# Kernel tuning notes

Measured on AMD Instinct MI355X. Metric: run time of the kernel, lower is better.

Reference implementation:

```python
import jax, jax.numpy as jnp
import numpy as np

B, S, T = 128, 128, 128
E, H = 256, 512
NEG_INF = -1e9


def setup_inputs() -> dict:
    key = jax.random.key(0)
    ks = jax.random.split(key, 12)
    rn = lambda k, sh: (jax.random.normal(k, sh, jnp.float32) * 0.05)
    return {
        "trg_embed": rn(ks[0], (B, T, E)),
        "encoder_hidden": rn(ks[1], (B, S, 2 * H)),
        "encoder_final": rn(ks[2], (1, B, 2 * H)),
        "src_mask": jnp.ones((B, 1, S), bool),
        "trg_mask": jnp.ones((B, T), bool),
        # Bahdanau attention params (Linear, bias=False)
        "W_key": rn(ks[3], (H, 2 * H)),      # key_layer
        "W_query": rn(ks[4], (H, H)),        # query_layer
        "v_energy": rn(ks[5], (H,)),         # energy_layer (H -> 1)
        # GRU cell params (torch layout: gates [r, z, n])
        "W_ih": rn(ks[6], (3 * H, E + 2 * H)),
        "W_hh": rn(ks[7], (3 * H, H)),
        "b_ih": rn(ks[8], (3 * H,)),
        "b_hh": rn(ks[9], (3 * H,)),
        # bridge: Linear(2H -> H, bias=True)
        "W_bridge": rn(ks[10], (H, 2 * H)),
        "b_bridge": jnp.zeros((H,), jnp.float32),
        # pre_output_layer: Linear(H + 2H + E -> H, bias=False)
        "W_preout": rn(ks[11], (H, H + 2 * H + E)),
    }


def reference(trg_embed, encoder_hidden, encoder_final, src_mask, trg_mask,
              W_key, W_query, v_energy, W_ih, W_hh, b_ih, b_hh,
              W_bridge, b_bridge, W_preout):
    # proj_key precomputed once, as in the torch module
    proj_key = jnp.einsum("bsk,hk->bsh", encoder_hidden, W_key)  # [B,S,H]
    # init_hidden: tanh(bridge(encoder_final)); num_layers=1 -> h: [B,H]
    h0 = jnp.tanh(encoder_final[0] @ W_bridge.T + b_bridge)
    mask = src_mask[:, 0, :]  # [B,S]

    def step(h, prev_embed):  # h: [B,H], prev_embed: [B,E]
        # Bahdanau additive attention, query = last-layer hidden
        q = h @ W_query.T  # [B,H]
        scores = jnp.einsum("bsh,h->bs", jnp.tanh(q[:, None, :] + proj_key), v_energy)
        scores = jnp.where(mask, scores, NEG_INF)
        alphas = jax.nn.softmax(scores, axis=-1)
        context = jnp.einsum("bs,bsd->bd", alphas, encoder_hidden)  # [B,2H]
        # single-step GRU (torch gate order r, z, n)
        x = jnp.concatenate([prev_embed, context], axis=-1)  # [B,E+2H]
        gi = x @ W_ih.T + b_ih
        gh = h @ W_hh.T + b_hh
        i_r, i_z, i_n = jnp.split(gi, 3, axis=-1)
        h_r, h_z, h_n = jnp.split(gh, 3, axis=-1)
        r = jax.nn.sigmoid(i_r + h_r)
        z = jax.nn.sigmoid(i_z + h_z)
        n = jnp.tanh(i_n + r * h_n)
        h_new = (1.0 - z) * n + z * h
        # pre-output projection (dropout p=0 / eval mode)
        pre = jnp.concatenate([prev_embed, h_new, context], axis=-1) @ W_preout.T
        return h_new, (h_new, pre)

    xs = jnp.swapaxes(trg_embed, 0, 1)  # [T,B,E]
    hT, (states, preouts) = jax.lax.scan(step, h0, xs)
    decoder_states = jnp.swapaxes(states, 0, 1)      # [B,T,H]
    pre_output_vectors = jnp.swapaxes(preouts, 0, 1)  # [B,T,H]
    hidden = hT[None]  # [1,B,H] to mirror torch layout
    cell_state = jnp.zeros_like(hidden)  # GRU: untouched zeros
    return decoder_states, hidden, pre_output_vectors, cell_state
```

## Files before the change

kernel.cpp:

```cpp
#include <hip/hip_runtime.h>
#include <hip/hip_bf16.h>

typedef __bf16 bf16_t;
typedef __bf16 bf16x8 __attribute__((ext_vector_type(8)));
typedef float  f32x4  __attribute__((ext_vector_type(4)));
typedef float  f32x2  __attribute__((ext_vector_type(2)));

#define Bx 128
#define Sx 128
#define Tx 128
#define Ex 256
#define Hx 512
#define H2 1024
#define G3 1536
#define KX 1280
#define KP 1792

#define OUT_STATES 0
#define OUT_HID    8388608
#define OUT_PRE    8454144
#define OUT_CELL   16842752

__device__ __forceinline__ float fast_tanh(float x){
  float e = __expf(2.0f*x);
  return 1.0f - 2.0f/(e + 1.0f);
}
__device__ __forceinline__ float fast_sigmoid(float x){
  return 1.0f/(1.0f + __expf(-x));
}

__device__ __forceinline__ bf16x8 ld_cvt8(const float* p){
  f32x4 a = *(const f32x4*)p;
  f32x4 b = *(const f32x4*)(p+4);
  bf16x8 r;
  r[0]=(bf16_t)a[0]; r[1]=(bf16_t)a[1]; r[2]=(bf16_t)a[2]; r[3]=(bf16_t)a[3];
  r[4]=(bf16_t)b[0]; r[5]=(bf16_t)b[1]; r[6]=(bf16_t)b[2]; r[7]=(bf16_t)b[3];
  return r;
}

__device__ __forceinline__ f32x4 gemm_tile_bb(const bf16_t* A, int lda,
                                              const bf16_t* W, int ldw, int K, int lane){
  const int quad = lane >> 4, c = lane & 15;
  const bf16_t* pa = A + c*lda + quad*8;
  const bf16_t* pb = W + c*ldw + quad*8;
  f32x4 acc = {0.f,0.f,0.f,0.f};
  for (int k = 0; k < K; k += 32)
    acc = __builtin_amdgcn_mfma_f32_16x16x32_bf16(*(const bf16x8*)(pa+k),
                                                  *(const bf16x8*)(pb+k), acc, 0, 0, 0);
  return acc;
}

__device__ __forceinline__ void store_tile_f32(float* C, int ldc, f32x4 acc, int lane){
  const int quad = lane >> 4, c = lane & 15;
  #pragma unroll
  for (int r = 0; r < 4; r++) C[(quad*4 + r)*ldc + c] = acc[r];
}

__global__ void cvt_kernel(const float* __restrict__ in, bf16_t* __restrict__ out, int n){
  const int i = (blockIdx.x*256 + threadIdx.x)*4;
  if (i < n){
    f32x4 v = *(const f32x4*)(in + i);
    bf16_t o[4]; o[0]=(bf16_t)v[0]; o[1]=(bf16_t)v[1]; o[2]=(bf16_t)v[2]; o[3]=(bf16_t)v[3];
    *(ulong1*)(out + i) = *(ulong1*)o;
  }
}

__global__ void bridge_kernel(const float* __restrict__ ef, const float* __restrict__ Wb,
                              const float* __restrict__ bb,
                              float* __restrict__ hf, bf16_t* __restrict__ hb){
  const int b = blockIdx.x;
  const int h = threadIdx.x;
  __shared__ float efs[H2];
  for (int k = threadIdx.x; k < H2; k += blockDim.x) efs[k] = ef[b*H2 + k];
  __syncthreads();
  const float* wrow = Wb + h*H2;
  float acc = bb[h];
  for (int k = 0; k < H2; k += 4){
    f32x4 w = *(const f32x4*)(wrow + k);
    acc += efs[k]*w[0] + efs[k+1]*w[1] + efs[k+2]*w[2] + efs[k+3]*w[3];
  }
  float v = fast_tanh(acc);
  hf[b*Hx + h] = v;
  hb[b*Hx + h] = (bf16_t)v;
}

__global__ void pk_gemm(const float* __restrict__ eh, const bf16_t* __restrict__ Wkb,
                        bf16_t* __restrict__ pk){
  const int gwid = (blockIdx.x*blockDim.x + threadIdx.x) >> 6;
  const int lane = threadIdx.x & 63;
  const int quad = lane >> 4, c = lane & 15;
  const int mt = gwid >> 5;
  const int nt = gwid & 31;
  const float*  pa = eh  + (mt*16 + c)*H2 + quad*8;
  const bf16_t* pb = Wkb + (nt*16 + c)*H2 + quad*8;
  f32x4 acc = {0.f,0.f,0.f,0.f};
  for (int k = 0; k < H2; k += 32)
    acc = __builtin_amdgcn_mfma_f32_16x16x32_bf16(ld_cvt8(pa + k),
                                                  *(const bf16x8*)(pb + k), acc, 0,0,0);
  bf16_t* C = pk + mt*16*Hx + nt*16;
  #pragma unroll
  for (int r = 0; r < 4; r++) C[(quad*4 + r)*Hx + c] = (bf16_t)acc[r];
}

__global__ void __launch_bounds__(256)
p1_kernel(const bf16_t* __restrict__ hb, const bf16_t* __restrict__ Wqb,
          const bf16_t* __restrict__ Whhb, float* __restrict__ qf, float* __restrict__ ghf){
  const int lane = threadIdx.x & 63;
  const int gw = blockIdx.x*4 + (threadIdx.x >> 6);
  if (gw < 256){
    const int mt = gw >> 5, nt = gw & 31;
    f32x4 acc = gemm_tile_bb(hb + mt*16*Hx, Hx, Wqb + nt*16*Hx, Hx, Hx, lane);
    store_tile_f32(qf + mt*16*Hx + nt*16, Hx, acc, lane);
  } else {
    const int idx = gw - 256;
    const int mt = idx/96, nt = idx%96;
    f32x4 acc = gemm_tile_bb(hb + mt*16*Hx, Hx, Whhb + nt*16*Hx, Hx, Hx, lane);
    store_tile_f32(ghf + mt*16*G3 + nt*16, G3, acc, lane);
  }
}

__global__ void __launch_bounds__(256)
p2_kernel(const float* __restrict__ trg, const float* __restrict__ eh,
          const float* __restrict__ ven, const bf16_t* __restrict__ pk,
          const float* __restrict__ qf, bf16_t* __restrict__ xbuf, int t){
  const int tid  = threadIdx.x;
  const int lane = tid & 63;
  const int wid  = tid >> 6;
  const int b    = blockIdx.x >> 1;
  const int half = blockIdx.x & 1;

  __shared__ float sc[Sx];
  __shared__ float smax_s, ssum_s;

  float qv[8], vv[8];
  #pragma unroll
  for (int i = 0; i < 8; i++){
    qv[i] = qf[b*Hx + i*64 + lane];
    vv[i] = ven[i*64 + lane];
  }
  for (int j = 0; j < 32; j++){
    const int s = wid*32 + j;
    const bf16_t* row = pk + (b*Sx + s)*Hx;
    float p = 0.f;
    #pragma unroll
    for (int i = 0; i < 8; i++)
      p += fast_tanh(qv[i] + (float)row[i*64 + lane])*vv[i];
    #pragma unroll
    for (int o = 32; o; o >>= 1) p += __shfl_xor(p, o, 64);
    if (lane == 0) sc[s] = p;
  }
  __syncthreads();
  if (tid < 64){
    float m = fmaxf(sc[tid], sc[tid+64]);
    #pragma unroll
    for (int o = 32; o; o >>= 1) m = fmaxf(m, __shfl_xor(m, o, 64));
    if (tid == 0) smax_s = m;
  }
  __syncthreads();
  if (tid < 128) sc[tid] = __expf(sc[tid] - smax_s);
  __syncthreads();
  if (tid < 64){
    float ssum = sc[tid] + sc[tid+64];
    #pragma unroll
    for (int o = 32; o; o >>= 1) ssum += __shfl_xor(ssum, o, 64);
    if (tid == 0) ssum_s = ssum;
  }
  __syncthreads();
  const float inv = 1.0f/ssum_s;
  const int d0 = half*Hx + tid*2;
  const float* ehb = eh + b*Sx*H2;
  float c0 = 0.f, c1 = 0.f;
  #pragma unroll 4
  for (int s = 0; s < Sx; s++){
    const float a = sc[s];
    f32x2 v = *(const f32x2*)(ehb + s*H2 + d0);
    c0 += a*v[0];
    c1 += a*v[1];
  }
  c0 *= inv; c1 *= inv;
  bf16_t cb[2]; cb[0] = (bf16_t)c0; cb[1] = (bf16_t)c1;
  *(uint1*)(xbuf + b*KX + Ex + d0) = *(uint1*)cb;
  if (half == 0) xbuf[b*KX + tid] = (bf16_t)trg[(b*Tx + t)*Ex + tid];
}

__global__ void __launch_bounds__(256)
p3_kernel(const bf16_t* __restrict__ Wihb, const float* __restrict__ bih,
          const float* __restrict__ bhh, const bf16_t* __restrict__ Wpb,
          const bf16_t* __restrict__ xbuf, const float* __restrict__ ghf,
          float* __restrict__ hf, bf16_t* __restrict__ hb,
          float* __restrict__ states, float* __restrict__ pre, int t){
  const int lane = threadIdx.x & 63;
  const int gw = blockIdx.x*4 + (threadIdx.x >> 6);
  const int quad = lane >> 4, c16 = lane & 15;

  if (gw < 256){
    const int mt = gw >> 5, ntp = gw & 31;
    const bf16_t* A  = xbuf + (mt*16 + c16)*KX + quad*8;
    const bf16_t* B0 = Wihb + (ntp*16 + c16)*KX + quad*8;
    const bf16_t* B1 = B0 + Hx*KX;
    const bf16_t* B2 = B0 + H2*KX;
    f32x4 ar = {0.f,0.f,0.f,0.f}, az = ar, an = ar;
    for (int k = 0; k < KX; k += 32){
      bf16x8 a = *(const bf16x8*)(A + k);
      ar = __builtin_amdgcn_mfma_f32_16x16x32_bf16(a, *(const bf16x8*)(B0+k), ar, 0,0,0);
      az = __builtin_amdgcn_mfma_f32_16x16x32_bf16(a, *(const bf16x8*)(B1+k), az, 0,0,0);
      an = __builtin_amdgcn_mfma_f32_16x16x32_bf16(a, *(const bf16x8*)(B2+k), an, 0,0,0);
    }
    const int j = ntp*16 + c16;
    const float bir = bih[j], biz = bih[Hx+j], bin = bih[H2+j];
    const float bhr = bhh[j], bhz = bhh[Hx+j], bhn = bhh[H2+j];
    #pragma unroll
    for (int r = 0; r < 4; r++){
      const int b_ = mt*16 + quad*4 + r;
      const float hr = ghf[b_*G3 + j]       + bhr;
      const float hz = ghf[b_*G3 + Hx + j]  + bhz;
      const float hn = ghf[b_*G3 + H2 + j]  + bhn;
      const float rg = fast_sigmoid(ar[r] + bir + hr);
      const float zg = fast_sigmoid(az[r] + biz + hz);
      const float ng = fast_tanh(an[r] + bin + rg*hn);
      const float hold = hf[b_*Hx + j];
      const float hnew = (1.0f - zg)*ng + zg*hold;
      hf[b_*Hx + j] = hnew;
      hb[b_*Hx + j] = (bf16_t)hnew;
      states[(b_*Tx + t)*Hx + j] = hnew;
    }
  } else {
    const int idx = gw - 256;
    const int mt2 = idx >> 5, nt2 = idx & 31;
    const bf16_t* A = xbuf + (mt2*16 + c16)*KX + Ex + quad*8;
    const bf16_t* B = Wpb + (nt2*16 + c16)*KP + (Ex + Hx) + quad*8;
    f32x4 acc = {0.f,0.f,0.f,0.f};
    for (int k = 0; k < H2; k += 32)
      acc = __builtin_amdgcn_mfma_f32_16x16x32_bf16(*(const bf16x8*)(A+k),
                                                    *(const bf16x8*)(B+k), acc, 0,0,0);
    #pragma unroll
    for (int r = 0; r < 4; r++){
      const int b_ = mt2*16 + quad*4 + r;
      pre[(b_*Tx + t)*Hx + nt2*16 + c16] = acc[r];
    }
  }
}

__global__ void preout_gemm(const bf16_t* __restrict__ trgb, const float* __restrict__ states,
                            const bf16_t* __restrict__ Wpb, float* __restrict__ pre){
  const int gwid = (blockIdx.x*blockDim.x + threadIdx.x) >> 6;
  const int lane = threadIdx.x & 63;
  const int quad = lane >> 4, c16 = lane & 15;
  const int mt = gwid >> 5, nt = gwid & 31;
  const int m = mt*16 + c16;
  const bf16_t* Bp = Wpb + (nt*16 + c16)*KP + quad*8;
  f32x4 acc = {0.f,0.f,0.f,0.f};
  const bf16_t* Ae = trgb + m*Ex + quad*8;
  for (int k = 0; k < Ex; k += 32)
    acc = __builtin_amdgcn_mfma_f32_16x16x32_bf16(*(const bf16x8*)(Ae+k),
                                                  *(const bf16x8*)(Bp+k), acc, 0,0,0);
  const float* As = states + m*Hx + quad*8;
  for (int k = 0; k < Hx; k += 32)
    acc = __builtin_amdgcn_mfma_f32_16x16x32_bf16(ld_cvt8(As+k),
                                                  *(const bf16x8*)(Bp+Ex+k), acc, 0,0,0);
  float* C = pre + mt*16*Hx + nt*16;
  #pragma unroll
  for (int r = 0; r < 4; r++){
    const int o = (quad*4 + r)*Hx + c16;
    C[o] = acc[r] + C[o];
  }
}

__global__ void finalize_kernel(const float* __restrict__ hf,
                                float* __restrict__ hid, float* __restrict__ cell){
  const int i = blockIdx.x*256 + threadIdx.x;
  hid[i]  = hf[i];
  cell[i] = 0.0f;
}

extern "C" void kernel_launch(void* const* d_in, const int* in_sizes, int n_in,
                              void* d_out, int out_size, void* d_ws, size_t ws_size,
                              hipStream_t stream){
  int shift = 0;
  for (int i = 0; i < n_in; i++){
    if (in_sizes[i] == 1966080){ shift = i - 8; break; }
  }
  #define IN(k) (((k) < 3) ? d_in[(k)] : d_in[(k) + shift])
  const float* trg = (const float*)IN(0);
  const float* eh  = (const float*)IN(1);
  const float* ef  = (const float*)IN(2);
  const float* Wk  = (const float*)IN(5);
  const float* Wq  = (const float*)IN(6);
  const float* ven = (const float*)IN(7);
  const float* Wih = (const float*)IN(8);
  const float* Whh = (const float*)IN(9);
  const float* bih = (const float*)IN(10);
  const float* bhh = (const float*)IN(11);
  const float* Wb  = (const float*)IN(12);
  const float* bb  = (const float*)IN(13);
  const float* Wp  = (const float*)IN(14);
  #undef IN

  char* ws = (char*)d_ws;
  bf16_t* xbuf = (bf16_t*)(ws + 0);
  float*  hf   = (float* )(ws + 327680);
  bf16_t* hb   = (bf16_t*)(ws + 589824);
  float*  qf   = (float* )(ws + 720896);
  float*  ghf  = (float* )(ws + 983040);
  bf16_t* Wkb  = (bf16_t*)(ws + 1769472);
  bf16_t* Wqb  = (bf16_t*)(ws + 2818048);
  bf16_t* Whhb = (bf16_t*)(ws + 3342336);
  bf16_t* Wihb = (bf16_t*)(ws + 4915200);
  bf16_t* Wpb  = (bf16_t*)(ws + 8847360);
  bf16_t* trgb = (bf16_t*)(ws + 10682368);
  bf16_t* pk   = (bf16_t*)(ws + 19070976);

  float* out    = (float*)d_out;
  float* states = out + OUT_STATES;
  float* hid    = out + OUT_HID;
  float* pre    = out + OUT_PRE;
  float* cell   = out + OUT_CELL;

  cvt_kernel<<<dim3(512),  dim3(256), 0, stream>>>(Wk,  Wkb,  524288);
  cvt_kernel<<<dim3(256),  dim3(256), 0, stream>>>(Wq,  Wqb,  262144);
  cvt_kernel<<<dim3(768),  dim3(256), 0, stream>>>(Whh, Whhb, 786432);
  cvt_kernel<<<dim3(1920), dim3(256), 0, stream>>>(Wih, Wihb, 1966080);
  cvt_kernel<<<dim3(896),  dim3(256), 0, stream>>>(Wp,  Wpb,  917504);
  cvt_kernel<<<dim3(4096), dim3(256), 0, stream>>>(trg, trgb, 4194304);

  bridge_kernel<<<dim3(Bx), dim3(Hx), 0, stream>>>(ef, Wb, bb, hf, hb);
  pk_gemm<<<dim3(8192), dim3(256), 0, stream>>>(eh, Wkb, pk);

  for (int t = 0; t < Tx; t++){
    p1_kernel<<<dim3(256), dim3(256), 0, stream>>>(hb, Wqb, Whhb, qf, ghf);
    p2_kernel<<<dim3(256), dim3(256), 0, stream>>>(trg, eh, ven, pk, qf, xbuf, t);
    p3_kernel<<<dim3(128), dim3(256), 0, stream>>>(Wihb, bih, bhh, Wpb, xbuf, ghf,
                                                   hf, hb, states, pre, t);
  }

  preout_gemm<<<dim3(8192), dim3(256), 0, stream>>>(trgb, states, Wpb, pre);
  finalize_kernel<<<dim3(256), dim3(256), 0, stream>>>(hf, hid, cell);
}
```

Baseline: 9.220 ms.

## Fuse per-timestep kernels into one persistent kernel with grid-wide barriers

Replaces the 384 per-step kernel launches (three phases across 128 timesteps) with a single persistent kernel of 256 blocks. The blocks step through all timesteps and separate the phases with an atomic-counter grid barrier. This is meant to remove launch overhead and inter-kernel gaps in the latency-bound recurrence. It relies on all 256 blocks being co-resident, and it borrows the cell output buffer as barrier storage; finalize later overwrites that buffer.

```diff
diff --git a/kernel.cpp b/kernel.cpp
--- a/kernel.cpp
+++ b/kernel.cpp
@@ -15,6 +15,8 @@
 #define G3 1536
 #define KX 1280
 #define KP 1792
+
+#define NBLK 256
 
 #define OUT_STATES 0
 #define OUT_HID    8388608
@@ -55,6 +57,26 @@
   #pragma unroll
   for (int r = 0; r < 4; r++) C[(quad*4 + r)*ldc + c] = acc[r];
 }
+
+__device__ __forceinline__ void gsync(unsigned* barv, unsigned next){
+  __syncthreads();
+  if (threadIdx.x == 0){
+    unsigned prev = __hip_atomic_fetch_add(&barv[0], 1u, __ATOMIC_ACQ_REL,
+                                           __HIP_MEMORY_SCOPE_AGENT);
+    if (prev == (unsigned)(NBLK - 1)){
+      __hip_atomic_store(&barv[0], 0u, __ATOMIC_RELAXED, __HIP_MEMORY_SCOPE_AGENT);
+      __hip_atomic_store(&barv[1], next, __ATOMIC_RELEASE, __HIP_MEMORY_SCOPE_AGENT);
+    } else {
+      while (__hip_atomic_load(&barv[1], __ATOMIC_RELAXED,
+                               __HIP_MEMORY_SCOPE_AGENT) != next)
+        __builtin_amdgcn_s_sleep(2);
+      __builtin_amdgcn_fence(__ATOMIC_ACQUIRE, "agent");
+    }
+  }
+  __syncthreads();
+}
+
+__global__ void init_bar(unsigned* barv){ barv[0] = 0u; barv[1] = 0u; }
 
 __global__ void cvt_kernel(const float* __restrict__ in, bf16_t* __restrict__ out, int n){
   const int i = (blockIdx.x*256 + threadIdx.x)*4;
@@ -103,141 +125,145 @@
 }
 
 __global__ void __launch_bounds__(256)
-p1_kernel(const bf16_t* __restrict__ hb, const bf16_t* __restrict__ Wqb,
-          const bf16_t* __restrict__ Whhb, float* __restrict__ qf, float* __restrict__ ghf){
-  const int lane = threadIdx.x & 63;
-  const int gw = blockIdx.x*4 + (threadIdx.x >> 6);
-  if (gw < 256){
-    const int mt = gw >> 5, nt = gw & 31;
-    f32x4 acc = gemm_tile_bb(hb + mt*16*Hx, Hx, Wqb + nt*16*Hx, Hx, Hx, lane);
-    store_tile_f32(qf + mt*16*Hx + nt*16, Hx, acc, lane);
-  } else {
-    const int idx = gw - 256;
-    const int mt = idx/96, nt = idx%96;
-    f32x4 acc = gemm_tile_bb(hb + mt*16*Hx, Hx, Whhb + nt*16*Hx, Hx, Hx, lane);
-    store_tile_f32(ghf + mt*16*G3 + nt*16, G3, acc, lane);
-  }
-}
-
-__global__ void __launch_bounds__(256)
-p2_kernel(const float* __restrict__ trg, const float* __restrict__ eh,
-          const float* __restrict__ ven, const bf16_t* __restrict__ pk,
-          const float* __restrict__ qf, bf16_t* __restrict__ xbuf, int t){
+loop_kernel(const float* __restrict__ trg, const float* __restrict__ eh,
+            const float* __restrict__ ven, const bf16_t* __restrict__ pk,
+            const bf16_t* __restrict__ Wqb, const bf16_t* __restrict__ Whhb,
+            const bf16_t* __restrict__ Wihb, const float* __restrict__ bih,
+            const float* __restrict__ bhh, const bf16_t* __restrict__ Wpb,
+            bf16_t* __restrict__ xbuf, float* __restrict__ qf, float* __restrict__ ghf,
+            float* __restrict__ hf, bf16_t* __restrict__ hb,
+            float* __restrict__ states, float* __restrict__ pre,
+            unsigned* __restrict__ barv){
   const int tid  = threadIdx.x;
   const int lane = tid & 63;
   const int wid  = tid >> 6;
-  const int b    = blockIdx.x >> 1;
-  const int half = blockIdx.x & 1;
+  const int blk  = blockIdx.x;
+  const int gw   = blk*4 + wid;
+  const int quad = lane >> 4, c16 = lane & 15;
+
+  const int b    = blk >> 1;
+  const int half = blk & 1;
+  const int d0   = half*Hx + tid*2;
+  const float* ehb = eh + b*Sx*H2;
 
   __shared__ float sc[Sx];
   __shared__ float smax_s, ssum_s;
 
-  float qv[8], vv[8];
+  float vv[8];
   #pragma unroll
-  for (int i = 0; i < 8; i++){
-    qv[i] = qf[b*Hx + i*64 + lane];
-    vv[i] = ven[i*64 + lane];
-  }
-  for (int j = 0; j < 32; j++){
-    const int s = wid*32 + j;
-    const bf16_t* row = pk + (b*Sx + s)*Hx;
-    float p = 0.f;
-    #pragma unroll
-    for (int i = 0; i < 8; i++)
-      p += fast_tanh(qv[i] + (float)row[i*64 + lane])*vv[i];
-    #pragma unroll
-    for (int o = 32; o; o >>= 1) p += __shfl_xor(p, o, 64);
-    if (lane == 0) sc[s] = p;
-  }
-  __syncthreads();
-  if (tid < 64){
-    float m = fmaxf(sc[tid], sc[tid+64]);
-    #pragma unroll
-    for (int o = 32; o; o >>= 1) m = fmaxf(m, __shfl_xor(m, o, 64));
-    if (tid == 0) smax_s = m;
-  }
-  __syncthreads();
-  if (tid < 128) sc[tid] = __expf(sc[tid] - smax_s);
-  __syncthreads();
-  if (tid < 64){
-    float ssum = sc[tid] + sc[tid+64];
-    #pragma unroll
-    for (int o = 32; o; o >>= 1) ssum += __shfl_xor(ssum, o, 64);
-    if (tid == 0) ssum_s = ssum;
-  }
-  __syncthreads();
-  const float inv = 1.0f/ssum_s;
-  const int d0 = half*Hx + tid*2;
-  const float* ehb = eh + b*Sx*H2;
-  float c0 = 0.f, c1 = 0.f;
-  #pragma unroll 4
-  for (int s = 0; s < Sx; s++){
-    const float a = sc[s];
-    f32x2 v = *(const f32x2*)(ehb + s*H2 + d0);
-    c0 += a*v[0];
-    c1 += a*v[1];
-  }
-  c0 *= inv; c1 *= inv;
-  bf16_t cb[2]; cb[0] = (bf16_t)c0; cb[1] = (bf16_t)c1;
-  *(uint1*)(xbuf + b*KX + Ex + d0) = *(uint1*)cb;
-  if (half == 0) xbuf[b*KX + tid] = (bf16_t)trg[(b*Tx + t)*Ex + tid];
-}
-
-__global__ void __launch_bounds__(256)
-p3_kernel(const bf16_t* __restrict__ Wihb, const float* __restrict__ bih,
-          const float* __restrict__ bhh, const bf16_t* __restrict__ Wpb,
-          const bf16_t* __restrict__ xbuf, const float* __restrict__ ghf,
-          float* __restrict__ hf, bf16_t* __restrict__ hb,
-          float* __restrict__ states, float* __restrict__ pre, int t){
-  const int lane = threadIdx.x & 63;
-  const int gw = blockIdx.x*4 + (threadIdx.x >> 6);
-  const int quad = lane >> 4, c16 = lane & 15;
-
-  if (gw < 256){
-    const int mt = gw >> 5, ntp = gw & 31;
-    const bf16_t* A  = xbuf + (mt*16 + c16)*KX + quad*8;
-    const bf16_t* B0 = Wihb + (ntp*16 + c16)*KX + quad*8;
-    const bf16_t* B1 = B0 + Hx*KX;
-    const bf16_t* B2 = B0 + H2*KX;
-    f32x4 ar = {0.f,0.f,0.f,0.f}, az = ar, an = ar;
-    for (int k = 0; k < KX; k += 32){
-      bf16x8 a = *(const bf16x8*)(A + k);
-      ar = __builtin_amdgcn_mfma_f32_16x16x32_bf16(a, *(const bf16x8*)(B0+k), ar, 0,0,0);
-      az = __builtin_amdgcn_mfma_f32_16x16x32_bf16(a, *(const bf16x8*)(B1+k), az, 0,0,0);
-      an = __builtin_amdgcn_mfma_f32_16x16x32_bf16(a, *(const bf16x8*)(B2+k), an, 0,0,0);
+  for (int i = 0; i < 8; i++) vv[i] = ven[i*64 + lane];
+
+  unsigned gen = 0;
+
+  for (int t = 0; t < Tx; t++){
+    if (gw < 256){
+      const int mt = gw >> 5, nt = gw & 31;
+      f32x4 acc = gemm_tile_bb(hb + mt*16*Hx, Hx, Wqb + nt*16*Hx, Hx, Hx, lane);
+      store_tile_f32(qf + mt*16*Hx + nt*16, Hx, acc, lane);
+    } else {
+      const int idx = gw - 256;
+      const int mt = idx/96, nt = idx%96;
+      f32x4 acc = gemm_tile_bb(hb + mt*16*Hx, Hx, Whhb + nt*16*Hx, Hx, Hx, lane);
+      store_tile_f32(ghf + mt*16*G3 + nt*16, G3, acc, lane);
     }
-    const int j = ntp*16 + c16;
-    const float bir = bih[j], biz = bih[Hx+j], bin = bih[H2+j];
-    const float bhr = bhh[j], bhz = bhh[Hx+j], bhn = bhh[H2+j];
-    #pragma unroll
-    for (int r = 0; r < 4; r++){
-      const int b_ = mt*16 + quad*4 + r;
-      const float hr = ghf[b_*G3 + j]       + bhr;
-      const float hz = ghf[b_*G3 + Hx + j]  + bhz;
-      const float hn = ghf[b_*G3 + H2 + j]  + bhn;
-      const float rg = fast_sigmoid(ar[r] + bir + hr);
-      const float zg = fast_sigmoid(az[r] + biz + hz);
-      const float ng = fast_tanh(an[r] + bin + rg*hn);
-      const float hold = hf[b_*Hx + j];
-      const float hnew = (1.0f - zg)*ng + zg*hold;
-      hf[b_*Hx + j] = hnew;
-      hb[b_*Hx + j] = (bf16_t)hnew;
-      states[(b_*Tx + t)*Hx + j] = hnew;
+    gsync(barv, ++gen);
+
+    {
+      float qv[8];
+      #pragma unroll
+      for (int i = 0; i < 8; i++) qv[i] = qf[b*Hx + i*64 + lane];
+
+      for (int j = 0; j < 32; j++){
+        const int s = wid*32 + j;
+        const bf16_t* row = pk + (b*Sx + s)*Hx;
+        float p = 0.f;
+        #pragma unroll
+        for (int i = 0; i < 8; i++)
+          p += fast_tanh(qv[i] + (float)row[i*64 + lane])*vv[i];
+        #pragma unroll
+        for (int o = 32; o; o >>= 1) p += __shfl_xor(p, o, 64);
+        if (lane == 0) sc[s] = p;
+      }
+      __syncthreads();
+      if (tid < 64){
+        float m = fmaxf(sc[tid], sc[tid+64]);
+        #pragma unroll
+        for (int o = 32; o; o >>= 1) m = fmaxf(m, __shfl_xor(m, o, 64));
+        if (tid == 0) smax_s = m;
+      }
+      __syncthreads();
+      if (tid < 128) sc[tid] = __expf(sc[tid] - smax_s);
+      __syncthreads();
+      if (tid < 64){
+        float ssum = sc[tid] + sc[tid+64];
+        #pragma unroll
+        for (int o = 32; o; o >>= 1) ssum += __shfl_xor(ssum, o, 64);
+        if (tid == 0) ssum_s = ssum;
+      }
+      __syncthreads();
+      const float inv = 1.0f/ssum_s;
+      float c0 = 0.f, c1 = 0.f;
+      #pragma unroll 4
+      for (int s = 0; s < Sx; s++){
+        const float a = sc[s];
+        f32x2 v = *(const f32x2*)(ehb + s*H2 + d0);
+        c0 += a*v[0];
+        c1 += a*v[1];
+      }
+      c0 *= inv; c1 *= inv;
+      bf16_t cb[2]; cb[0] = (bf16_t)c0; cb[1] = (bf16_t)c1;
+      *(uint1*)(xbuf + b*KX + Ex + d0) = *(uint1*)cb;
+      if (half == 0) xbuf[b*KX + tid] = (bf16_t)trg[(b*Tx + t)*Ex + tid];
     }
-  } else {
-    const int idx = gw - 256;
-    const int mt2 = idx >> 5, nt2 = idx & 31;
-    const bf16_t* A = xbuf + (mt2*16 + c16)*KX + Ex + quad*8;
-    const bf16_t* B = Wpb + (nt2*16 + c16)*KP + (Ex + Hx) + quad*8;
-    f32x4 acc = {0.f,0.f,0.f,0.f};
-    for (int k = 0; k < H2; k += 32)
-      acc = __builtin_amdgcn_mfma_f32_16x16x32_bf16(*(const bf16x8*)(A+k),
-                                                    *(const bf16x8*)(B+k), acc, 0,0,0);
-    #pragma unroll
-    for (int r = 0; r < 4; r++){
-      const int b_ = mt2*16 + quad*4 + r;
-      pre[(b_*Tx + t)*Hx + nt2*16 + c16] = acc[r];
+    gsync(barv, ++gen);
+
+    if (gw < 256){
+      const int mt = gw >> 5, ntp = gw & 31;
+      const bf16_t* A  = xbuf + (mt*16 + c16)*KX + quad*8;
+      const bf16_t* B0 = Wihb + (ntp*16 + c16)*KX + quad*8;
+      const bf16_t* B1 = B0 + Hx*KX;
+      const bf16_t* B2 = B0 + H2*KX;
+      f32x4 ar = {0.f,0.f,0.f,0.f}, az = ar, an = ar;
+      for (int k = 0; k < KX; k += 32){
+        bf16x8 a = *(const bf16x8*)(A + k);
+        ar = __builtin_amdgcn_mfma_f32_16x16x32_bf16(a, *(const bf16x8*)(B0+k), ar, 0,0,0);
+        az = __builtin_amdgcn_mfma_f32_16x16x32_bf16(a, *(const bf16x8*)(B1+k), az, 0,0,0);
+        an = __builtin_amdgcn_mfma_f32_16x16x32_bf16(a, *(const bf16x8*)(B2+k), an, 0,0,0);
+      }
+      const int j = ntp*16 + c16;
+      const float bir = bih[j], biz = bih[Hx+j], bin = bih[H2+j];
+      const float bhr = bhh[j], bhz = bhh[Hx+j], bhn = bhh[H2+j];
+      #pragma unroll
+      for (int r = 0; r < 4; r++){
+        const int b_ = mt*16 + quad*4 + r;
+        const float hr = ghf[b_*G3 + j]       + bhr;
+        const float hz = ghf[b_*G3 + Hx + j]  + bhz;
+        const float hn = ghf[b_*G3 + H2 + j]  + bhn;
+        const float rg = fast_sigmoid(ar[r] + bir + hr);
+        const float zg = fast_sigmoid(az[r] + biz + hz);
+        const float ng = fast_tanh(an[r] + bin + rg*hn);
+        const float hold = hf[b_*Hx + j];
+        const float hnew = (1.0f - zg)*ng + zg*hold;
+        hf[b_*Hx + j] = hnew;
+        hb[b_*Hx + j] = (bf16_t)hnew;
+        states[(b_*Tx + t)*Hx + j] = hnew;
+      }
+    } else if (gw < 512){
+      const int idx = gw - 256;
+      const int mt2 = idx >> 5, nt2 = idx & 31;
+      const bf16_t* A = xbuf + (mt2*16 + c16)*KX + Ex + quad*8;
+      const bf16_t* B = Wpb + (nt2*16 + c16)*KP + (Ex + Hx) + quad*8;
+      f32x4 acc = {0.f,0.f,0.f,0.f};
+      for (int k = 0; k < H2; k += 32)
+        acc = __builtin_amdgcn_mfma_f32_16x16x32_bf16(*(const bf16x8*)(A+k),
+                                                      *(const bf16x8*)(B+k), acc, 0,0,0);
+      #pragma unroll
+      for (int r = 0; r < 4; r++){
+        const int b_ = mt2*16 + quad*4 + r;
+        pre[(b_*Tx + t)*Hx + nt2*16 + c16] = acc[r];
+      }
     }
+    gsync(barv, ++gen);
   }
 }
 
@@ -316,6 +342,8 @@
   float* pre    = out + OUT_PRE;
   float* cell   = out + OUT_CELL;
 
+  unsigned* barv = (unsigned*)cell;
+
   cvt_kernel<<<dim3(512),  dim3(256), 0, stream>>>(Wk,  Wkb,  524288);
   cvt_kernel<<<dim3(256),  dim3(256), 0, stream>>>(Wq,  Wqb,  262144);
   cvt_kernel<<<dim3(768),  dim3(256), 0, stream>>>(Whh, Whhb, 786432);
@@ -325,13 +353,12 @@
 
   bridge_kernel<<<dim3(Bx), dim3(Hx), 0, stream>>>(ef, Wb, bb, hf, hb);
   pk_gemm<<<dim3(8192), dim3(256), 0, stream>>>(eh, Wkb, pk);
-
-  for (int t = 0; t < Tx; t++){
-    p1_kernel<<<dim3(256), dim3(256), 0, stream>>>(hb, Wqb, Whhb, qf, ghf);
-    p2_kernel<<<dim3(256), dim3(256), 0, stream>>>(trg, eh, ven, pk, qf, xbuf, t);
-    p3_kernel<<<dim3(128), dim3(256), 0, stream>>>(Wihb, bih, bhh, Wpb, xbuf, ghf,
-                                                   hf, hb, states, pre, t);
-  }
+  init_bar<<<dim3(1), dim3(1), 0, stream>>>(barv);
+
+  loop_kernel<<<dim3(NBLK), dim3(256), 0, stream>>>(trg, eh, ven, pk,
+                                                    Wqb, Whhb, Wihb, bih, bhh, Wpb,
+                                                    xbuf, qf, ghf, hf, hb,
+                                                    states, pre, barv);
 
   preout_gemm<<<dim3(8192), dim3(256), 0, stream>>>(trgb, states, Wpb, pre);
   finalize_kernel<<<dim3(256), dim3(256), 0, stream>>>(hf, hid, cell);
```

New measurement: 16.41 ms. 1.78x slower.
